# Kernel tuning notes

Measured on AMD Instinct MI355X. Metric: run time of the kernel, lower is better.

Reference implementation:

```python
import jax, jax.numpy as jnp
import numpy as np

N_HEAD = 16
D_MODEL = 1024
D_K = 64
D_V = 64
LN_EPS = 1e-6


def setup_inputs() -> dict:
    key = jax.random.key(0)
    ks = jax.random.split(key, 10)
    B, S = 2, 2048
    scale = 0.02
    return {
        "q": jax.random.normal(ks[0], (B, S, D_MODEL), jnp.float32),
        "k": jax.random.normal(ks[1], (B, S, D_MODEL), jnp.float32),
        "v": jax.random.normal(ks[2], (B, S, D_MODEL), jnp.float32),
        "Wq": jax.random.normal(ks[3], (D_MODEL, N_HEAD * D_K), jnp.float32) * scale,
        "Wk": jax.random.normal(ks[4], (D_MODEL, N_HEAD * D_K), jnp.float32) * scale,
        "Wv": jax.random.normal(ks[5], (D_MODEL, N_HEAD * D_V), jnp.float32) * scale,
        "Wfc": jax.random.normal(ks[6], (N_HEAD * D_V, D_MODEL), jnp.float32) * scale,
        "bfc": jnp.zeros((D_MODEL,), jnp.float32),
        "gamma": jnp.ones((D_MODEL,), jnp.float32),
        "beta": jnp.zeros((D_MODEL,), jnp.float32),
    }


def reference(q, k, v, Wq, Wk, Wv, Wfc, bfc, gamma, beta):
    B, S, _ = q.shape
    residual = q
    # QKV projections, split into heads: [B, S, H, Dh]
    qh = (q @ Wq).reshape(B, S, N_HEAD, D_K)
    kh = (k @ Wk).reshape(B, S, N_HEAD, D_K)
    vh = (v @ Wv).reshape(B, S, N_HEAD, D_V)
    # scaled dot-product attention (explicit score matrix, as in source)
    temperature = jnp.asarray(D_K, qh.dtype) ** 0.5
    attn = jnp.einsum("bqhd,bkhd->bhqk", qh, kh) / temperature
    attn = jax.nn.softmax(attn, axis=-1)
    out = jnp.einsum("bhqk,bkhd->bqhd", attn, vh).reshape(B, S, N_HEAD * D_V)
    # output projection (dropout is identity in eval mode)
    out = out @ Wfc + bfc
    # residual + layernorm (eps=1e-6)
    x = out + residual
    mu = jnp.mean(x, axis=-1, keepdims=True)
    var = jnp.mean(jnp.square(x - mu), axis=-1, keepdims=True)
    return (x - mu) / jnp.sqrt(var + LN_EPS) * gamma + beta
```

## Files before the change

### kernel.cpp

```cpp
#include <hip/hip_runtime.h>

typedef float f32x4 __attribute__((ext_vector_type(4)));
typedef short short8 __attribute__((ext_vector_type(8)));
typedef short short4v __attribute__((ext_vector_type(4)));
typedef unsigned int uint2v __attribute__((ext_vector_type(2)));
typedef unsigned short ushort_t;

#define D_MODEL 1024
#define N_HEAD 16
#define SEQ 2048
#define BATCH 2
#define M_TOK 4096
#define HD 1024
#define NT 32
#define APANEL 131072
#define WPANEL 32768
#define QSCALE_L2E 0.1803368801111f

__device__ __forceinline__ ushort_t f2bf(float f) {
    union { float f; unsigned int u; } x; x.f = f;
    unsigned int r = x.u + 0x7fffu + ((x.u >> 16) & 1u);
    return (ushort_t)(r >> 16);
}

__device__ __forceinline__ void async_copy16(const ushort_t* gptr, ushort_t* lptr) {
    __builtin_amdgcn_global_load_lds(
        (const __attribute__((address_space(1))) unsigned int*)gptr,
        (__attribute__((address_space(3))) unsigned int*)lptr, 16, 0, 0);
}

__global__ __launch_bounds__(256) void prep_fused(const float* __restrict__ w0,
                                                  const float* __restrict__ w1,
                                                  const float* __restrict__ w2,
                                                  const float* __restrict__ w3,
                                                  ushort_t* __restrict__ o0,
                                                  ushort_t* __restrict__ o1,
                                                  ushort_t* __restrict__ o2,
                                                  ushort_t* __restrict__ o3,
                                                  const float* __restrict__ q,
                                                  const float* __restrict__ k,
                                                  const float* __restrict__ v,
                                                  ushort_t* __restrict__ qo,
                                                  ushort_t* __restrict__ ko,
                                                  ushort_t* __restrict__ vo) {
    const int z = blockIdx.z;
    const int tid = threadIdx.x;
    const int flat = blockIdx.x + 64 * blockIdx.y;
    if (z < 4) {
        if (flat >= 1024) return;
        const int C = D_MODEL;
        const float* in = (z == 0) ? w0 : (z == 1) ? w1 : (z == 2) ? w2 : w3;
        ushort_t* out = (z == 0) ? o0 : (z == 1) ? o1 : (z == 2) ? o2 : o3;
        __shared__ ushort_t t[32][33];
        int bc = (flat & 31) * 32, br = (flat >> 5) * 32;
        int tx = tid & 31, ty = tid >> 5;
        for (int i = ty; i < 32; i += 8)
            t[i][tx] = f2bf(in[(size_t)(br + i) * C + bc + tx]);
        __syncthreads();
        size_t pbase = (size_t)(br >> 5) * WPANEL;
        for (int i = ty; i < 32; i += 8)
            out[pbase + (size_t)(bc + i) * 32 + tx] = t[tx][i];
    } else {
        const float* s = (z == 4) ? q : (z == 5) ? k : v;
        ushort_t* d = (z == 4) ? qo : (z == 5) ? ko : vo;
        size_t i = ((size_t)flat * 256 + tid) * 8;
        int m = (int)(i >> 10), k0 = (int)(i & 1023);
        float4 a = *(const float4*)(s + i);
        float4 b = *(const float4*)(s + i + 4);
        ushort_t tmp[8] = {f2bf(a.x), f2bf(a.y), f2bf(a.z), f2bf(a.w),
                           f2bf(b.x), f2bf(b.y), f2bf(b.z), f2bf(b.w)};
        *(short8*)(d + (size_t)(k0 >> 5) * APANEL + (size_t)m * 32 + (k0 & 31)) = *(short8*)tmp;
    }
}

__global__ __launch_bounds__(256) void gemm_qkv(const ushort_t* __restrict__ qb,
                                                const ushort_t* __restrict__ kb,
                                                const ushort_t* __restrict__ vb,
                                                const ushort_t* __restrict__ wq,
                                                const ushort_t* __restrict__ wk,
                                                const ushort_t* __restrict__ wv,
                                                ushort_t* __restrict__ Qo,
                                                ushort_t* __restrict__ Ko,
                                                ushort_t* __restrict__ V4) {
    __shared__ ushort_t As[2][128 * 32];
    __shared__ ushort_t Bs[2][128 * 32];
    const int z = blockIdx.z;
    const ushort_t* A = (z == 0) ? qb : (z == 1) ? kb : vb;
    const ushort_t* Bt = (z == 0) ? wq : (z == 1) ? wk : wv;
    const int tid = threadIdx.x;
    const int wave = tid >> 6, lane = tid & 63;
    const int quad = lane >> 4, l16 = lane & 15;
    const int m0 = blockIdx.x * 128, n0 = blockIdx.y * 128;
    const int wm = (wave >> 1) * 64, wn = (wave & 1) * 64;
    const int N = D_MODEL;

    f32x4 acc[4][4];
    for (int i = 0; i < 4; ++i)
        for (int j = 0; j < 4; ++j) acc[i][j] = (f32x4){0.f, 0.f, 0.f, 0.f};

    for (int it = 0; it < 16; ++it) {
        __syncthreads();
        const ushort_t* Ap = A + (size_t)(it * 2) * APANEL + (size_t)m0 * 32;
        const ushort_t* Bp = Bt + (size_t)(it * 2) * WPANEL + (size_t)n0 * 32;
        #pragma unroll
        for (int hf = 0; hf < 2; ++hf) {
            #pragma unroll
            for (int c = 0; c < 2; ++c) {
                int off = (wave * 2 + c) * 512;
                async_copy16(Ap + hf * APANEL + off + lane * 8, &As[hf][off] + lane * 8);
                async_copy16(Bp + hf * WPANEL + off + lane * 8, &Bs[hf][off] + lane * 8);
            }
        }
        __syncthreads();
        short8 af[4][2], bfr[4][2];
        #pragma unroll
        for (int i = 0; i < 4; ++i)
            #pragma unroll
            for (int sk = 0; sk < 2; ++sk)
                af[i][sk] = *(const short8*)&As[sk][(wm + i * 16 + l16) * 32 + quad * 8];
        #pragma unroll
        for (int j = 0; j < 4; ++j)
            #pragma unroll
            for (int sk = 0; sk < 2; ++sk)
                bfr[j][sk] = *(const short8*)&Bs[sk][(wn + j * 16 + l16) * 32 + quad * 8];
        #pragma unroll
        for (int sk = 0; sk < 2; ++sk)
            #pragma unroll
            for (int i = 0; i < 4; ++i)
                #pragma unroll
                for (int j = 0; j < 4; ++j)
                    acc[i][j] = __builtin_amdgcn_mfma_f32_16x16x32_bf16(af[i][sk], bfr[j][sk], acc[i][j], 0, 0, 0);
    }
    if (z == 2) {
        const int tile64 = m0 + wm;
        const int b2 = tile64 >> 11;
        const int kt = (tile64 & 2047) >> 6;
        #pragma unroll
        for (int i = 0; i < 4; ++i)
            #pragma unroll
            for (int j = 0; j < 4; ++j) {
                int n = n0 + wn + j * 16 + l16;
                int h2 = n >> 6, d = n & 63;
                int quadR = (quad + ((n >> 2) & 3)) & 3;
                ushort_t tmp[4];
                #pragma unroll
                for (int r = 0; r < 4; ++r) tmp[r] = f2bf(acc[i][j][r]);
                size_t dst = ((((size_t)(h2 * 2 + b2) * NT + kt) * 4 + i) << 10) + d * 16 + quadR * 4;
                *(short4v*)&V4[dst] = *(short4v*)tmp;
            }
    } else {
        ushort_t* C = (z == 0) ? Qo : Ko;
        const float scale = (z == 0) ? QSCALE_L2E : 1.0f;
        #pragma unroll
        for (int i = 0; i < 4; ++i)
            #pragma unroll
            for (int j = 0; j < 4; ++j) {
                int n = n0 + wn + j * 16 + l16;
                #pragma unroll
                for (int r = 0; r < 4; ++r) {
                    int m = m0 + wm + i * 16 + quad * 4 + r;
                    C[(size_t)m * N + n] = f2bf(acc[i][j][r] * scale);
                }
            }
    }
}

__global__ __launch_bounds__(256) void gemm_fc(const ushort_t* __restrict__ A,
                                               const ushort_t* __restrict__ Bt,
                                               float* __restrict__ Cf,
                                               const float* __restrict__ bias,
                                               const float* __restrict__ resid) {
    __shared__ ushort_t As[2][128 * 32];
    __shared__ ushort_t Bs[2][64 * 32];
    const int tid = threadIdx.x;
    const int wave = tid >> 6, lane = tid & 63;
    const int quad = lane >> 4, l16 = lane & 15;
    const int m0 = blockIdx.x * 128, n0 = blockIdx.y * 64;
    const int N = D_MODEL;

    f32x4 acc[2][4];
    for (int i = 0; i < 2; ++i)
        for (int j = 0; j < 4; ++j) acc[i][j] = (f32x4){0.f, 0.f, 0.f, 0.f};

    for (int it = 0; it < 16; ++it) {
        __syncthreads();
        const ushort_t* Ap = A + (size_t)(it * 2) * APANEL + (size_t)m0 * 32;
        const ushort_t* Bp = Bt + (size_t)(it * 2) * WPANEL + (size_t)n0 * 32;
        #pragma unroll
        for (int c = 0; c < 4; ++c) {
            int g = wave * 4 + c;
            int sk = g >> 3, off = (g & 7) * 512;
            async_copy16(Ap + sk * APANEL + off + lane * 8, &As[sk][off] + lane * 8);
        }
        #pragma unroll
        for (int c = 0; c < 2; ++c) {
            int g = wave * 2 + c;
            int sk = g >> 2, off = (g & 3) * 512;
            async_copy16(Bp + sk * WPANEL + off + lane * 8, &Bs[sk][off] + lane * 8);
        }
        __syncthreads();
        short8 af[2][2], bfr[4][2];
        #pragma unroll
        for (int i = 0; i < 2; ++i)
            #pragma unroll
            for (int sk = 0; sk < 2; ++sk)
                af[i][sk] = *(const short8*)&As[sk][(wave * 32 + i * 16 + l16) * 32 + quad * 8];
        #pragma unroll
        for (int j = 0; j < 4; ++j)
            #pragma unroll
            for (int sk = 0; sk < 2; ++sk)
                bfr[j][sk] = *(const short8*)&Bs[sk][(j * 16 + l16) * 32 + quad * 8];
        #pragma unroll
        for (int sk = 0; sk < 2; ++sk)
            #pragma unroll
            for (int i = 0; i < 2; ++i)
                #pragma unroll
                for (int j = 0; j < 4; ++j)
                    acc[i][j] = __builtin_amdgcn_mfma_f32_16x16x32_bf16(af[i][sk], bfr[j][sk], acc[i][j], 0, 0, 0);
    }
    #pragma unroll
    for (int i = 0; i < 2; ++i)
        #pragma unroll
        for (int j = 0; j < 4; ++j) {
            int n = n0 + j * 16 + l16;
            #pragma unroll
            for (int r = 0; r < 4; ++r) {
                int m = m0 + wave * 32 + i * 16 + quad * 4 + r;
                Cf[(size_t)m * N + n] = acc[i][j][r] + bias[n] + resid[(size_t)m * N + n];
            }
        }
}

__global__ __launch_bounds__(256, 3) void attn64(const ushort_t* __restrict__ Qh,
                                                 const ushort_t* __restrict__ Kh,
                                                 const ushort_t* __restrict__ V4,
                                                 ushort_t* __restrict__ O) {
    __shared__ __align__(16) char smem[25600];
    const int tid = threadIdx.x;
    const int wave = tid >> 6, lane = tid & 63;
    const int quad = lane >> 4, l16 = lane & 15;
    const int h = blockIdx.x, b = blockIdx.y, qt = blockIdx.z;
    const size_t base = (size_t)b * SEQ * HD + h * 64;
    const ushort_t* Qb = Qh + base + (size_t)(qt * 64) * HD;
    const ushort_t* Kb = Kh + base;
    const ushort_t* Vg = V4 + (((size_t)(h * 2 + b) * NT * 4) + wave) * 1024 + lane * 8;

    ushort_t* Vw = (ushort_t*)smem + wave * 3072;
    float* lsb = (float*)(smem + 24576);

    short8 qf[4][2];
    #pragma unroll
    for (int nt = 0; nt < 4; ++nt)
        #pragma unroll
        for (int s = 0; s < 2; ++s)
            qf[nt][s] = *(const short8*)(Qb + (size_t)(nt * 16 + l16) * HD + s * 32 + quad * 8);

    f32x4 oacc[4][4];
    #pragma unroll
    for (int nt = 0; nt < 4; ++nt)
        #pragma unroll
        for (int dt = 0; dt < 4; ++dt) oacc[nt][dt] = (f32x4){0.f, 0.f, 0.f, 0.f};
    float lsum[4] = {0.f, 0.f, 0.f, 0.f};

    const ushort_t* Kr = Kb + (size_t)(wave * 16 + l16) * HD + quad * 8;
    ushort_t* VLd = Vw + lane * 8;

    short8 kf0[2], kf1[2];
    #pragma unroll
    for (int s = 0; s < 2; ++s) kf0[s] = *(const short8*)(Kr + s * 32);
    #pragma unroll
    for (int c = 0; c < 2; ++c) async_copy16(Vg + c * 512, VLd + c * 512);
    #pragma unroll
    for (int c = 0; c < 2; ++c) async_copy16(Vg + 4096 + c * 512, VLd + 1024 + c * 512);

    ushort_t *vb0 = Vw, *vb1 = Vw + 1024, *vb2 = Vw + 2048;
    const int rot = (l16 >> 2) & 3;

    for (int kt = 0; kt < NT; ++kt) {
        if (kt == NT - 1) __builtin_amdgcn_s_waitcnt(0x0F70);
        else              __builtin_amdgcn_s_waitcnt(0x0F72);

        if (kt + 1 < NT) {
            #pragma unroll
            for (int s = 0; s < 2; ++s)
                kf1[s] = *(const short8*)(Kr + (size_t)(kt + 1) * 64 * HD + s * 32);
        }
        if (kt + 2 < NT) {
            #pragma unroll
            for (int c = 0; c < 2; ++c)
                async_copy16(Vg + (size_t)(kt + 2) * 4096 + c * 512, vb2 + lane * 8 + c * 512);
        }

        short4v vf[4];
        #pragma unroll
        for (int dt = 0; dt < 4; ++dt)
            vf[dt] = *(const short4v*)&vb0[(dt * 16 + l16) * 16 + (((quad + rot) & 3) * 4)];

        f32x4 sacc[4];
        #pragma unroll
        for (int nt = 0; nt < 4; ++nt) sacc[nt] = (f32x4){0.f, 0.f, 0.f, 0.f};
        #pragma unroll
        for (int s = 0; s < 2; ++s)
            #pragma unroll
            for (int nt = 0; nt < 4; ++nt)
                sacc[nt] = __builtin_amdgcn_mfma_f32_16x16x32_bf16(kf0[s], qf[nt][s], sacc[nt], 0, 0, 0);

        short4v pf[4];
        #pragma unroll
        for (int nt = 0; nt < 4; ++nt) {
            float p0 = __builtin_amdgcn_exp2f(sacc[nt][0]);
            float p1 = __builtin_amdgcn_exp2f(sacc[nt][1]);
            float p2 = __builtin_amdgcn_exp2f(sacc[nt][2]);
            float p3 = __builtin_amdgcn_exp2f(sacc[nt][3]);
            lsum[nt] += (p0 + p1) + (p2 + p3);
            unsigned int lo, hi;
            asm("v_cvt_pk_bf16_f32 %0, %1, %2" : "=v"(lo) : "v"(p0), "v"(p1));
            asm("v_cvt_pk_bf16_f32 %0, %1, %2" : "=v"(hi) : "v"(p2), "v"(p3));
            uint2v pk;
            pk.x = lo;
            pk.y = hi;
            pf[nt] = __builtin_bit_cast(short4v, pk);
        }
        #pragma unroll
        for (int nt = 0; nt < 4; ++nt)
            #pragma unroll
            for (int dt = 0; dt < 4; ++dt)
                oacc[nt][dt] = __builtin_amdgcn_mfma_f32_16x16x16bf16_1k(pf[nt], vf[dt], oacc[nt][dt], 0, 0, 0);

        kf0[0] = kf1[0]; kf0[1] = kf1[1];
        ushort_t* t = vb0; vb0 = vb1; vb1 = vb2; vb2 = t;
    }

    #pragma unroll
    for (int nt = 0; nt < 4; ++nt) {
        lsum[nt] += __shfl_xor(lsum[nt], 16, 64);
        lsum[nt] += __shfl_xor(lsum[nt], 32, 64);
    }
    if (quad == 0) {
        #pragma unroll
        for (int nt = 0; nt < 4; ++nt) lsb[wave * 64 + nt * 16 + l16] = lsum[nt];
    }
    __syncthreads();

    float* R = (float*)smem;
    #pragma unroll
    for (int w = 0; w < 4; ++w) {
        if (wave == w) {
            #pragma unroll
            for (int nt = 0; nt < 4; ++nt)
                #pragma unroll
                for (int dt = 0; dt < 4; ++dt)
                    #pragma unroll
                    for (int i = 0; i < 4; ++i) {
                        int idx = (nt * 16 + quad * 4 + i) * 66 + dt * 16 + l16;
                        if (w == 0) R[idx] = oacc[nt][dt][i];
                        else        R[idx] += oacc[nt][dt][i];
                    }
        }
        __syncthreads();
    }
    float inv[4];
    #pragma unroll
    for (int i = 0; i < 4; ++i) {
        int qrow = wave * 16 + quad * 4 + i;
        float t = lsb[qrow] + lsb[64 + qrow] + lsb[128 + qrow] + lsb[192 + qrow];
        inv[i] = 1.f / t;
    }
    #pragma unroll
    for (int i = 0; i < 4; ++i) {
        int qrow = wave * 16 + quad * 4 + i;
        size_t tok = (size_t)b * SEQ + qt * 64 + qrow;
        #pragma unroll
        for (int dt = 0; dt < 4; ++dt) {
            int d = dt * 16 + l16;
            size_t dst = (size_t)(h * 2 + (dt >> 1)) * APANEL + tok * 32 + (dt & 1) * 16 + l16;
            O[dst] = f2bf(R[qrow * 66 + d] * inv[i]);
        }
    }
}

__global__ __launch_bounds__(256) void ln_kernel(float* __restrict__ x,
                                                 const float* __restrict__ gamma,
                                                 const float* __restrict__ beta) {
    const int D = D_MODEL;
    float* xr = x + (size_t)blockIdx.x * D;
    const int tid = threadIdx.x;
    float4 v = *(const float4*)(xr + tid * 4);
    float s = v.x + v.y + v.z + v.w;
    float s2 = v.x * v.x + v.y * v.y + v.z * v.z + v.w * v.w;
    #pragma unroll
    for (int off = 1; off < 64; off <<= 1) {
        s += __shfl_xor(s, off, 64);
        s2 += __shfl_xor(s2, off, 64);
    }
    __shared__ float ws1[4], ws2[4];
    int wave = tid >> 6, lane = tid & 63;
    if (lane == 0) { ws1[wave] = s; ws2[wave] = s2; }
    __syncthreads();
    s = ws1[0] + ws1[1] + ws1[2] + ws1[3];
    s2 = ws2[0] + ws2[1] + ws2[2] + ws2[3];
    float mean = s * (1.f / D);
    float var = s2 * (1.f / D) - mean * mean;
    float rstd = rsqrtf(var + 1e-6f);
    float4 g = *(const float4*)(gamma + tid * 4);
    float4 bt = *(const float4*)(beta + tid * 4);
    float4 o;
    o.x = (v.x - mean) * rstd * g.x + bt.x;
    o.y = (v.y - mean) * rstd * g.y + bt.y;
    o.z = (v.z - mean) * rstd * g.z + bt.z;
    o.w = (v.w - mean) * rstd * g.w + bt.w;
    *(float4*)(xr + tid * 4) = o;
}

extern "C" void kernel_launch(void* const* d_in, const int* in_sizes, int n_in,
                              void* d_out, int out_size, void* d_ws, size_t ws_size,
                              hipStream_t stream) {
    const float* q = (const float*)d_in[0];
    const float* k = (const float*)d_in[1];
    const float* v = (const float*)d_in[2];
    const float* Wq = (const float*)d_in[3];
    const float* Wk = (const float*)d_in[4];
    const float* Wv = (const float*)d_in[5];
    const float* Wfc = (const float*)d_in[6];
    const float* bfc = (const float*)d_in[7];
    const float* gamma = (const float*)d_in[8];
    const float* beta = (const float*)d_in[9];
    float* out = (float*)d_out;

    char* ws = (char*)d_ws;
    const size_t MB = 1u << 20;
    ushort_t* WqT  = (ushort_t*)(ws + 0 * MB);
    ushort_t* WkT  = (ushort_t*)(ws + 2 * MB);
    ushort_t* WvT  = (ushort_t*)(ws + 4 * MB);
    ushort_t* WfcT = (ushort_t*)(ws + 6 * MB);
    ushort_t* qb   = (ushort_t*)(ws + 8 * MB);
    ushort_t* kb   = (ushort_t*)(ws + 16 * MB);
    ushort_t* vb   = (ushort_t*)(ws + 24 * MB);
    ushort_t* Qh   = (ushort_t*)(ws + 32 * MB);
    ushort_t* Kh   = (ushort_t*)(ws + 40 * MB);
    ushort_t* Vt   = (ushort_t*)(ws + 48 * MB);
    ushort_t* Oh   = (ushort_t*)(ws + 8 * MB);

    const int M = M_TOK, D = D_MODEL;
    prep_fused<<<dim3(64, 32, 7), 256, 0, stream>>>(
        Wq, Wk, Wv, Wfc, WqT, WkT, WvT, WfcT, q, k, v, qb, kb, vb);

    gemm_qkv<<<dim3(M / 128, D / 128, 3), 256, 0, stream>>>(qb, kb, vb, WqT, WkT, WvT, Qh, Kh, Vt);

    attn64<<<dim3(N_HEAD, BATCH, SEQ / 64), 256, 0, stream>>>(Qh, Kh, Vt, Oh);

    gemm_fc<<<dim3(M / 128, D / 64), 256, 0, stream>>>(Oh, WfcT, out, bfc, q);

    ln_kernel<<<M, 256, 0, stream>>>(out, gamma, beta);
}
```

Baseline: 240.1 us.

## Fuse fp32-to-bf16 activation conversion into QKV GEMM via fp32 LDS staging

Removes the separate pass that converted q/k/v activations to bf16 panel layout. The QKV GEMM now async-copies fp32 rows straight into shared memory with an XOR swizzle and converts them to bf16 with v_cvt_pk_bf16_f32 when building MFMA fragments. This drops one full read and write of the three 16 MB activation tensors plus their rereads. In exchange the GEMM loads twice as many bytes per A tile, uses more LDS, and repeats the conversion for every N-block that reads the same rows.

```diff
diff --git a/kernel.cpp b/kernel.cpp
--- a/kernel.cpp
+++ b/kernel.cpp
@@ -4,6 +4,7 @@
 typedef short short8 __attribute__((ext_vector_type(8)));
 typedef short short4v __attribute__((ext_vector_type(4)));
 typedef unsigned int uint2v __attribute__((ext_vector_type(2)));
+typedef unsigned int uint4v __attribute__((ext_vector_type(4)));
 typedef unsigned short ushort_t;
 
 #define D_MODEL 1024
@@ -23,7 +24,7 @@
     return (ushort_t)(r >> 16);
 }
 
-__device__ __forceinline__ void async_copy16(const ushort_t* gptr, ushort_t* lptr) {
+__device__ __forceinline__ void async_copy16(const void* gptr, void* lptr) {
     __builtin_amdgcn_global_load_lds(
         (const __attribute__((address_space(1))) unsigned int*)gptr,
         (__attribute__((address_space(3))) unsigned int*)lptr, 16, 0, 0);
@@ -36,56 +37,37 @@
                                                   ushort_t* __restrict__ o0,
                                                   ushort_t* __restrict__ o1,
                                                   ushort_t* __restrict__ o2,
-                                                  ushort_t* __restrict__ o3,
-                                                  const float* __restrict__ q,
-                                                  const float* __restrict__ k,
-                                                  const float* __restrict__ v,
-                                                  ushort_t* __restrict__ qo,
-                                                  ushort_t* __restrict__ ko,
-                                                  ushort_t* __restrict__ vo) {
+                                                  ushort_t* __restrict__ o3) {
     const int z = blockIdx.z;
     const int tid = threadIdx.x;
-    const int flat = blockIdx.x + 64 * blockIdx.y;
-    if (z < 4) {
-        if (flat >= 1024) return;
-        const int C = D_MODEL;
-        const float* in = (z == 0) ? w0 : (z == 1) ? w1 : (z == 2) ? w2 : w3;
-        ushort_t* out = (z == 0) ? o0 : (z == 1) ? o1 : (z == 2) ? o2 : o3;
-        __shared__ ushort_t t[32][33];
-        int bc = (flat & 31) * 32, br = (flat >> 5) * 32;
-        int tx = tid & 31, ty = tid >> 5;
-        for (int i = ty; i < 32; i += 8)
-            t[i][tx] = f2bf(in[(size_t)(br + i) * C + bc + tx]);
-        __syncthreads();
-        size_t pbase = (size_t)(br >> 5) * WPANEL;
-        for (int i = ty; i < 32; i += 8)
-            out[pbase + (size_t)(bc + i) * 32 + tx] = t[tx][i];
-    } else {
-        const float* s = (z == 4) ? q : (z == 5) ? k : v;
-        ushort_t* d = (z == 4) ? qo : (z == 5) ? ko : vo;
-        size_t i = ((size_t)flat * 256 + tid) * 8;
-        int m = (int)(i >> 10), k0 = (int)(i & 1023);
-        float4 a = *(const float4*)(s + i);
-        float4 b = *(const float4*)(s + i + 4);
-        ushort_t tmp[8] = {f2bf(a.x), f2bf(a.y), f2bf(a.z), f2bf(a.w),
-                           f2bf(b.x), f2bf(b.y), f2bf(b.z), f2bf(b.w)};
-        *(short8*)(d + (size_t)(k0 >> 5) * APANEL + (size_t)m * 32 + (k0 & 31)) = *(short8*)tmp;
-    }
-}
-
-__global__ __launch_bounds__(256) void gemm_qkv(const ushort_t* __restrict__ qb,
-                                                const ushort_t* __restrict__ kb,
-                                                const ushort_t* __restrict__ vb,
+    const int flat = blockIdx.x + 32 * blockIdx.y;
+    const int C = D_MODEL;
+    const float* in = (z == 0) ? w0 : (z == 1) ? w1 : (z == 2) ? w2 : w3;
+    ushort_t* out = (z == 0) ? o0 : (z == 1) ? o1 : (z == 2) ? o2 : o3;
+    __shared__ ushort_t t[32][33];
+    int bc = (flat & 31) * 32, br = (flat >> 5) * 32;
+    int tx = tid & 31, ty = tid >> 5;
+    for (int i = ty; i < 32; i += 8)
+        t[i][tx] = f2bf(in[(size_t)(br + i) * C + bc + tx]);
+    __syncthreads();
+    size_t pbase = (size_t)(br >> 5) * WPANEL;
+    for (int i = ty; i < 32; i += 8)
+        out[pbase + (size_t)(bc + i) * 32 + tx] = t[tx][i];
+}
+
+__global__ __launch_bounds__(256) void gemm_qkv(const float* __restrict__ qX,
+                                                const float* __restrict__ kX,
+                                                const float* __restrict__ vX,
                                                 const ushort_t* __restrict__ wq,
                                                 const ushort_t* __restrict__ wk,
                                                 const ushort_t* __restrict__ wv,
                                                 ushort_t* __restrict__ Qo,
                                                 ushort_t* __restrict__ Ko,
                                                 ushort_t* __restrict__ V4) {
-    __shared__ ushort_t As[2][128 * 32];
+    __shared__ float Af[2][128 * 32];
     __shared__ ushort_t Bs[2][128 * 32];
     const int z = blockIdx.z;
-    const ushort_t* A = (z == 0) ? qb : (z == 1) ? kb : vb;
+    const float* X = (z == 0) ? qX : (z == 1) ? kX : vX;
     const ushort_t* Bt = (z == 0) ? wq : (z == 1) ? wk : wv;
     const int tid = threadIdx.x;
     const int wave = tid >> 6, lane = tid & 63;
@@ -100,14 +82,22 @@
 
     for (int it = 0; it < 16; ++it) {
         __syncthreads();
-        const ushort_t* Ap = A + (size_t)(it * 2) * APANEL + (size_t)m0 * 32;
+        const float* Xp = X + (size_t)m0 * 1024 + it * 64;
         const ushort_t* Bp = Bt + (size_t)(it * 2) * WPANEL + (size_t)n0 * 32;
+        #pragma unroll
+        for (int c = 0; c < 8; ++c) {
+            int g = wave * 8 + c;
+            int sk = g >> 4, ch = g & 15;
+            int row = ch * 8 + (lane >> 3);
+            int swz = (lane & 7) ^ (row & 6);
+            async_copy16(Xp + (size_t)row * 1024 + sk * 32 + swz * 4,
+                         &Af[sk][ch * 256 + lane * 4]);
+        }
         #pragma unroll
         for (int hf = 0; hf < 2; ++hf) {
             #pragma unroll
             for (int c = 0; c < 2; ++c) {
                 int off = (wave * 2 + c) * 512;
-                async_copy16(Ap + hf * APANEL + off + lane * 8, &As[hf][off] + lane * 8);
                 async_copy16(Bp + hf * WPANEL + off + lane * 8, &Bs[hf][off] + lane * 8);
             }
         }
@@ -116,8 +106,20 @@
         #pragma unroll
         for (int i = 0; i < 4; ++i)
             #pragma unroll
-            for (int sk = 0; sk < 2; ++sk)
-                af[i][sk] = *(const short8*)&As[sk][(wm + i * 16 + l16) * 32 + quad * 8];
+            for (int sk = 0; sk < 2; ++sk) {
+                int row = wm + i * 16 + l16;
+                const float* fp = &Af[sk][row * 32 + (((quad * 2) ^ (row & 6)) * 4)];
+                float4 u0 = *(const float4*)fp;
+                float4 u1 = *(const float4*)(fp + 4);
+                unsigned int c0, c1, c2, c3;
+                asm("v_cvt_pk_bf16_f32 %0, %1, %2" : "=v"(c0) : "v"(u0.x), "v"(u0.y));
+                asm("v_cvt_pk_bf16_f32 %0, %1, %2" : "=v"(c1) : "v"(u0.z), "v"(u0.w));
+                asm("v_cvt_pk_bf16_f32 %0, %1, %2" : "=v"(c2) : "v"(u1.x), "v"(u1.y));
+                asm("v_cvt_pk_bf16_f32 %0, %1, %2" : "=v"(c3) : "v"(u1.z), "v"(u1.w));
+                uint4v pk4;
+                pk4.x = c0; pk4.y = c1; pk4.z = c2; pk4.w = c3;
+                af[i][sk] = __builtin_bit_cast(short8, pk4);
+            }
         #pragma unroll
         for (int j = 0; j < 4; ++j)
             #pragma unroll
@@ -433,19 +435,15 @@
     ushort_t* WkT  = (ushort_t*)(ws + 2 * MB);
     ushort_t* WvT  = (ushort_t*)(ws + 4 * MB);
     ushort_t* WfcT = (ushort_t*)(ws + 6 * MB);
-    ushort_t* qb   = (ushort_t*)(ws + 8 * MB);
-    ushort_t* kb   = (ushort_t*)(ws + 16 * MB);
-    ushort_t* vb   = (ushort_t*)(ws + 24 * MB);
+    ushort_t* Oh   = (ushort_t*)(ws + 8 * MB);
     ushort_t* Qh   = (ushort_t*)(ws + 32 * MB);
     ushort_t* Kh   = (ushort_t*)(ws + 40 * MB);
     ushort_t* Vt   = (ushort_t*)(ws + 48 * MB);
-    ushort_t* Oh   = (ushort_t*)(ws + 8 * MB);
 
     const int M = M_TOK, D = D_MODEL;
-    prep_fused<<<dim3(64, 32, 7), 256, 0, stream>>>(
-        Wq, Wk, Wv, Wfc, WqT, WkT, WvT, WfcT, q, k, v, qb, kb, vb);
-
-    gemm_qkv<<<dim3(M / 128, D / 128, 3), 256, 0, stream>>>(qb, kb, vb, WqT, WkT, WvT, Qh, Kh, Vt);
+    prep_fused<<<dim3(32, 32, 4), 256, 0, stream>>>(Wq, Wk, Wv, Wfc, WqT, WkT, WvT, WfcT);
+
+    gemm_qkv<<<dim3(M / 128, D / 128, 3), 256, 0, stream>>>(q, k, v, WqT, WkT, WvT, Qh, Kh, Vt);
 
     attn64<<<dim3(N_HEAD, BATCH, SEQ / 64), 256, 0, stream>>>(Qh, Kh, Vt, Oh);
 
```

After: 253.4 us. +5.5%, slower.

## Double-buffer LDS in QKV and FC GEMMs to overlap loads with MFMA

Applied to the files above, without the earlier changes.

The QKV and output-projection GEMMs now prefetch the next K panel into an alternate LDS buffer while computing on the current one. Each iteration handles one 32-wide K slice (32 iterations) instead of loading two slices and then waiting. This hides global-to-LDS latency behind the MFMA work, at the cost of twice as many loop iterations and barriers per block. Correctness depends on async_copy16 completing before the trailing __syncthreads, which the definition not shown must provide.

```diff
diff --git a/kernel.cpp b/kernel.cpp
--- a/kernel.cpp
+++ b/kernel.cpp
@@ -98,38 +98,43 @@
     for (int i = 0; i < 4; ++i)
         for (int j = 0; j < 4; ++j) acc[i][j] = (f32x4){0.f, 0.f, 0.f, 0.f};
 
-    for (int it = 0; it < 16; ++it) {
-        __syncthreads();
-        const ushort_t* Ap = A + (size_t)(it * 2) * APANEL + (size_t)m0 * 32;
-        const ushort_t* Bp = Bt + (size_t)(it * 2) * WPANEL + (size_t)n0 * 32;
-        #pragma unroll
-        for (int hf = 0; hf < 2; ++hf) {
+    const ushort_t* Ab = A + (size_t)m0 * 32;
+    const ushort_t* Bb = Bt + (size_t)n0 * 32;
+
+    #pragma unroll
+    for (int c = 0; c < 2; ++c) {
+        int off = (wave * 2 + c) * 512;
+        async_copy16(Ab + off + lane * 8, &As[0][off] + lane * 8);
+        async_copy16(Bb + off + lane * 8, &Bs[0][off] + lane * 8);
+    }
+    __syncthreads();
+
+    int cur = 0;
+    for (int it = 0; it < 32; ++it) {
+        if (it + 1 < 32) {
+            const ushort_t* Ap = Ab + (size_t)(it + 1) * APANEL;
+            const ushort_t* Bp = Bb + (size_t)(it + 1) * WPANEL;
             #pragma unroll
             for (int c = 0; c < 2; ++c) {
                 int off = (wave * 2 + c) * 512;
-                async_copy16(Ap + hf * APANEL + off + lane * 8, &As[hf][off] + lane * 8);
-                async_copy16(Bp + hf * WPANEL + off + lane * 8, &Bs[hf][off] + lane * 8);
+                async_copy16(Ap + off + lane * 8, &As[cur ^ 1][off] + lane * 8);
+                async_copy16(Bp + off + lane * 8, &Bs[cur ^ 1][off] + lane * 8);
             }
         }
+        short8 af[4], bfr[4];
+        #pragma unroll
+        for (int i = 0; i < 4; ++i)
+            af[i] = *(const short8*)&As[cur][(wm + i * 16 + l16) * 32 + quad * 8];
+        #pragma unroll
+        for (int j = 0; j < 4; ++j)
+            bfr[j] = *(const short8*)&Bs[cur][(wn + j * 16 + l16) * 32 + quad * 8];
+        #pragma unroll
+        for (int i = 0; i < 4; ++i)
+            #pragma unroll
+            for (int j = 0; j < 4; ++j)
+                acc[i][j] = __builtin_amdgcn_mfma_f32_16x16x32_bf16(af[i], bfr[j], acc[i][j], 0, 0, 0);
         __syncthreads();
-        short8 af[4][2], bfr[4][2];
-        #pragma unroll
-        for (int i = 0; i < 4; ++i)
-            #pragma unroll
-            for (int sk = 0; sk < 2; ++sk)
-                af[i][sk] = *(const short8*)&As[sk][(wm + i * 16 + l16) * 32 + quad * 8];
-        #pragma unroll
-        for (int j = 0; j < 4; ++j)
-            #pragma unroll
-            for (int sk = 0; sk < 2; ++sk)
-                bfr[j][sk] = *(const short8*)&Bs[sk][(wn + j * 16 + l16) * 32 + quad * 8];
-        #pragma unroll
-        for (int sk = 0; sk < 2; ++sk)
-            #pragma unroll
-            for (int i = 0; i < 4; ++i)
-                #pragma unroll
-                for (int j = 0; j < 4; ++j)
-                    acc[i][j] = __builtin_amdgcn_mfma_f32_16x16x32_bf16(af[i][sk], bfr[j][sk], acc[i][j], 0, 0, 0);
+        cur ^= 1;
     }
     if (z == 2) {
         const int tile64 = m0 + wm;
@@ -182,41 +187,43 @@
     for (int i = 0; i < 2; ++i)
         for (int j = 0; j < 4; ++j) acc[i][j] = (f32x4){0.f, 0.f, 0.f, 0.f};
 
-    for (int it = 0; it < 16; ++it) {
+    const ushort_t* Ab = A + (size_t)m0 * 32;
+    const ushort_t* Bb = Bt + (size_t)n0 * 32;
+
+    #pragma unroll
+    for (int c = 0; c < 2; ++c) {
+        int off = (wave * 2 + c) * 512;
+        async_copy16(Ab + off + lane * 8, &As[0][off] + lane * 8);
+    }
+    async_copy16(Bb + wave * 512 + lane * 8, &Bs[0][wave * 512] + lane * 8);
+    __syncthreads();
+
+    int cur = 0;
+    for (int it = 0; it < 32; ++it) {
+        if (it + 1 < 32) {
+            const ushort_t* Ap = Ab + (size_t)(it + 1) * APANEL;
+            const ushort_t* Bp = Bb + (size_t)(it + 1) * WPANEL;
+            #pragma unroll
+            for (int c = 0; c < 2; ++c) {
+                int off = (wave * 2 + c) * 512;
+                async_copy16(Ap + off + lane * 8, &As[cur ^ 1][off] + lane * 8);
+            }
+            async_copy16(Bp + wave * 512 + lane * 8, &Bs[cur ^ 1][wave * 512] + lane * 8);
+        }
+        short8 af[2], bfr[4];
+        #pragma unroll
+        for (int i = 0; i < 2; ++i)
+            af[i] = *(const short8*)&As[cur][(wave * 32 + i * 16 + l16) * 32 + quad * 8];
+        #pragma unroll
+        for (int j = 0; j < 4; ++j)
+            bfr[j] = *(const short8*)&Bs[cur][(j * 16 + l16) * 32 + quad * 8];
+        #pragma unroll
+        for (int i = 0; i < 2; ++i)
+            #pragma unroll
+            for (int j = 0; j < 4; ++j)
+                acc[i][j] = __builtin_amdgcn_mfma_f32_16x16x32_bf16(af[i], bfr[j], acc[i][j], 0, 0, 0);
         __syncthreads();
-        const ushort_t* Ap = A + (size_t)(it * 2) * APANEL + (size_t)m0 * 32;
-        const ushort_t* Bp = Bt + (size_t)(it * 2) * WPANEL + (size_t)n0 * 32;
-        #pragma unroll
-        for (int c = 0; c < 4; ++c) {
-            int g = wave * 4 + c;
-            int sk = g >> 3, off = (g & 7) * 512;
-            async_copy16(Ap + sk * APANEL + off + lane * 8, &As[sk][off] + lane * 8);
-        }
-        #pragma unroll
-        for (int c = 0; c < 2; ++c) {
-            int g = wave * 2 + c;
-            int sk = g >> 2, off = (g & 3) * 512;
-            async_copy16(Bp + sk * WPANEL + off + lane * 8, &Bs[sk][off] + lane * 8);
-        }
-        __syncthreads();
-        short8 af[2][2], bfr[4][2];
-        #pragma unroll
-        for (int i = 0; i < 2; ++i)
-            #pragma unroll
-            for (int sk = 0; sk < 2; ++sk)
-                af[i][sk] = *(const short8*)&As[sk][(wave * 32 + i * 16 + l16) * 32 + quad * 8];
-        #pragma unroll
-        for (int j = 0; j < 4; ++j)
-            #pragma unroll
-            for (int sk = 0; sk < 2; ++sk)
-                bfr[j][sk] = *(const short8*)&Bs[sk][(j * 16 + l16) * 32 + quad * 8];
-        #pragma unroll
-        for (int sk = 0; sk < 2; ++sk)
-            #pragma unroll
-            for (int i = 0; i < 2; ++i)
-                #pragma unroll
-                for (int j = 0; j < 4; ++j)
-                    acc[i][j] = __builtin_amdgcn_mfma_f32_16x16x32_bf16(af[i][sk], bfr[j][sk], acc[i][j], 0, 0, 0);
+        cur ^= 1;
     }
     #pragma unroll
     for (int i = 0; i < 2; ++i)
```

New measurement: 243.4 us. No clear change (+1.4%).
